# Kernel optimization log

Measured on AMD Instinct MI355X. Metric: run time of the kernel, lower is better.

## Reference

```python
import jax, jax.numpy as jnp
import numpy as np

K = 7          # kernel_size
PAD = 3        # padding
EPS = 1e-8


def setup_inputs() -> dict:
    key = jax.random.key(0)
    x = jax.random.normal(key, (32, 3, 512, 512), dtype=jnp.float32)
    return {"x": x}


def reference(x) -> jnp.ndarray:
    # Faithful fused version of: unfold -> center/neighbor cosine distance -> sum/8.
    # stride=1, dilation=1, padding=3, kernel=7 => output spatial size == input size,
    # and the patch center (flat index 24) is exactly the unpadded pixel itself.
    B, C, H, W = x.shape
    xp = jnp.pad(x, ((0, 0), (0, 0), (PAD, PAD), (PAD, PAD)))
    center = x  # == xp[:, :, PAD:PAD+H, PAD:PAD+W]
    # ||center|| over channels, clamped (matches .norm(dim=1).clamp_min(eps))
    cn = jnp.maximum(jnp.sqrt(jnp.sum(center * center, axis=1)), EPS)  # (B,H,W)
    acc = jnp.zeros((B, H, W), dtype=x.dtype)
    mid = K // 2
    for i in range(K):  # small fixed 7x7 loop; avoids materializing (B,C,49,H*W)
        for j in range(K):
            if i == mid and j == mid:
                continue  # skip center (neighbor_idx excludes center_flat)
            nb = xp[:, :, i:i + H, j:j + W]                      # (B,C,H,W)
            dot = jnp.sum(center * nb, axis=1)                   # (B,H,W)
            nn_ = jnp.maximum(jnp.sqrt(jnp.sum(nb * nb, axis=1)), EPS)
            acc = acc + (1.0 - dot / (cn * nn_))
    out = acc / 8.0  # module hardcodes /8 despite 48 neighbors
    return out[:, None, :, :]  # (B,1,H,W)
```

## Files before the change

### kernel.cpp

```cpp
#include <hip/hip_runtime.h>


typedef unsigned int u32;
typedef float f32x2 __attribute__((ext_vector_type(2)));
typedef float f32x4 __attribute__((ext_vector_type(4)));

#define EPS2 1e-16f

constexpr int HRN = 22;

__device__ __forceinline__ u32 packbf2(float a, float b) {
    const u32 ua = __float_as_uint(a) + 0x8000u;
    const u32 ub = __float_as_uint(b) + 0x8000u;
    return __builtin_amdgcn_perm(ub, ua, 0x07060302u);
}
__device__ __forceinline__ float uplo(u32 u) { return __uint_as_float(u << 16); }
__device__ __forceinline__ float uphi(u32 u) { return __uint_as_float(u & 0xffff0000u); }
__device__ __forceinline__ f32x2 up2(u32 u) {
    f32x2 r; r.x = uplo(u); r.y = uphi(u); return r;
}
__device__ __forceinline__ f32x4 vmul(f32x4 v, float s) {
    f32x4 r; r[0]=v[0]*s; r[1]=v[1]*s; r[2]=v[2]*s; r[3]=v[3]*s; return r;
}

__global__ __launch_bounds__(256, 3) void mcnd_kernel(const float* __restrict__ x,
                                                      float* __restrict__ out,
                                                      int B, int H, int W) {
    __shared__ uint4 hsh[4][3][HRN][8];

    const int HW = H * W;
    const int tilesX = W >> 6;
    const int tilesPerImg = tilesX * (H >> 6);

    const int cpx  = gridDim.x >> 3;
    const int wgid = (blockIdx.x & 7) * cpx + (blockIdx.x >> 3);
    const int b    = wgid / tilesPerImg;
    const int t    = wgid % tilesPerImg;
    const int ty   = t / tilesX;
    const int tx   = t - ty * tilesX;
    const int x0   = tx << 6;

    const int wv   = threadIdx.x >> 6;
    const int lane = threadIdx.x & 63;
    const int r2   = lane >> 3;
    const int grp  = lane & 7;
    const int yw   = (ty << 6) + (wv << 4);

    const float* __restrict__ xb = x + (size_t)b * 3 * HW;

    const int   gxl   = x0 + (grp << 3) - 4;
    const float lmask = (gxl >= 0) ? 1.f : 0.f;
    const float rmask = (gxl + 16 <= W) ? 1.f : 0.f;
    const int   gofL  = (gxl >= 0) ? gxl : 0;
    const int   gofR  = (gxl + 16 <= W) ? (gxl + 12) : (W - 4);

    u32 gA0[4], gA1[4], gA2[4];
    u32 gB0[4], gB1[4], gB2[4];
    uint4 hA[3], hB[3];

    auto process = [&](int hr, u32* cp0, u32* cp1, u32* cp2, uint4* hcap) {
        const int   gy  = yw + hr - 3;
        const float rmk = (gy >= 0 && gy < H) ? 1.f : 0.f;
        const int   gyc = gy < 0 ? 0 : (gy >= H ? H - 1 : gy);
        const float* rp0 = xb + (size_t)gyc * W;
        const float* rp1 = rp0 + HW;
        const float* rp2 = rp1 + HW;
        f32x4 a0 = *(const f32x4*)(rp0 + gofL);
        f32x4 a1 = *(const f32x4*)(rp0 + gxl + 4);
        f32x4 a2 = *(const f32x4*)(rp0 + gxl + 8);
        f32x4 a3 = *(const f32x4*)(rp0 + gofR);
        f32x4 b0 = *(const f32x4*)(rp1 + gofL);
        f32x4 b1 = *(const f32x4*)(rp1 + gxl + 4);
        f32x4 b2 = *(const f32x4*)(rp1 + gxl + 8);
        f32x4 b3 = *(const f32x4*)(rp1 + gofR);
        f32x4 c0 = *(const f32x4*)(rp2 + gofL);
        f32x4 c1 = *(const f32x4*)(rp2 + gxl + 4);
        f32x4 c2 = *(const f32x4*)(rp2 + gxl + 8);
        f32x4 c3 = *(const f32x4*)(rp2 + gofR);
        a0 = vmul(a0, lmask); b0 = vmul(b0, lmask); c0 = vmul(c0, lmask);
        a3 = vmul(a3, rmask); b3 = vmul(b3, rmask); c3 = vmul(c3, rmask);
        f32x4 i0, i1, i2, i3;
        {
            const f32x4 n0 = a0*a0 + b0*b0 + c0*c0;
            const f32x4 n1 = a1*a1 + b1*b1 + c1*c1;
            const f32x4 n2 = a2*a2 + b2*b2 + c2*c2;
            const f32x4 n3 = a3*a3 + b3*b3 + c3*c3;
#pragma unroll
            for (int e = 0; e < 4; ++e) {
                i0[e] = __builtin_amdgcn_rsqf(fmaxf(n0[e], EPS2)) * rmk;
                i1[e] = __builtin_amdgcn_rsqf(fmaxf(n1[e], EPS2)) * rmk;
                i2[e] = __builtin_amdgcn_rsqf(fmaxf(n2[e], EPS2)) * rmk;
                i3[e] = __builtin_amdgcn_rsqf(fmaxf(n3[e], EPS2)) * rmk;
            }
        }
        auto chan = [&](const f32x4& A0, const f32x4& A1, const f32x4& A2,
                        const f32x4& A3, int ch, u32* gcp, uint4* hc) {
            float cc[16];
#pragma unroll
            for (int e = 0; e < 4; ++e) {
                cc[e]      = A0[e] * i0[e];
                cc[4 + e]  = A1[e] * i1[e];
                cc[8 + e]  = A2[e] * i2[e];
                cc[12 + e] = A3[e] * i3[e];
            }
            float hp[8];
            hp[0] = cc[1]+cc[2]+cc[3]+cc[4]+cc[5]+cc[6]+cc[7];
#pragma unroll
            for (int m = 1; m < 8; ++m) hp[m] = hp[m-1] - cc[m] + cc[m+7];
            uint4 hwv;
            hwv.x = packbf2(hp[0], hp[1]); hwv.y = packbf2(hp[2], hp[3]);
            hwv.z = packbf2(hp[4], hp[5]); hwv.w = packbf2(hp[6], hp[7]);
            hsh[wv][ch][hr][grp] = hwv;
            if (hc) *hc = hwv;
            if (gcp) {
                gcp[0] = packbf2(cc[4],  cc[5]);
                gcp[1] = packbf2(cc[6],  cc[7]);
                gcp[2] = packbf2(cc[8],  cc[9]);
                gcp[3] = packbf2(cc[10], cc[11]);
            }
        };
        chan(a0, a1, a2, a3, 0, cp0, hcap ? &hcap[0] : nullptr);
        chan(b0, b1, b2, b3, 1, cp1, hcap ? &hcap[1] : nullptr);
        chan(c0, c1, c2, c3, 2, cp2, hcap ? &hcap[2] : nullptr);
    };

    process(2*r2 + 3, gA0, gA1, gA2, hA);
    process(2*r2 + 4, gB0, gB1, gB2, hB);
    if (lane < 48) {
        const int rr = lane >> 3;
        process(rr < 3 ? rr : rr + 16, nullptr, nullptr, nullptr, nullptr);
    }
    asm volatile("s_waitcnt lgkmcnt(0)" ::: "memory");
    __builtin_amdgcn_sched_barrier(0);

    f32x2 D0[4], D1[4];
#pragma unroll
    for (int e = 0; e < 4; ++e) { D0[e] = f32x2{0.f,0.f}; D1[e] = f32x2{0.f,0.f}; }
    auto vch = [&](int ch, const u32* ga, const u32* gb) {
        const uint4 u0 = hsh[wv][ch][2*r2][grp];
        f32x2 s0 = up2(u0.x), s1 = up2(u0.y), s2 = up2(u0.z), s3 = up2(u0.w);
#pragma unroll
        for (int d = 1; d < 3; ++d) {
            const uint4 u = hsh[wv][ch][2*r2 + d][grp];
            s0 += up2(u.x); s1 += up2(u.y); s2 += up2(u.z); s3 += up2(u.w);
        }
        s0 += up2(hA[ch].x) + up2(hB[ch].x);
        s1 += up2(hA[ch].y) + up2(hB[ch].y);
        s2 += up2(hA[ch].z) + up2(hB[ch].z);
        s3 += up2(hA[ch].w) + up2(hB[ch].w);
#pragma unroll
        for (int d = 5; d < 7; ++d) {
            const uint4 u = hsh[wv][ch][2*r2 + d][grp];
            s0 += up2(u.x); s1 += up2(u.y); s2 += up2(u.z); s3 += up2(u.w);
        }
        const uint4 u7 = hsh[wv][ch][2*r2 + 7][grp];
        D0[0] += up2(ga[0]) * s0;
        D0[1] += up2(ga[1]) * s1;
        D0[2] += up2(ga[2]) * s2;
        D0[3] += up2(ga[3]) * s3;
        D1[0] += up2(gb[0]) * (s0 - up2(u0.x) + up2(u7.x));
        D1[1] += up2(gb[1]) * (s1 - up2(u0.y) + up2(u7.y));
        D1[2] += up2(gb[2]) * (s2 - up2(u0.z) + up2(u7.z));
        D1[3] += up2(gb[3]) * (s3 - up2(u0.w) + up2(u7.w));
    };
    vch(0, gA0, gB0); vch(1, gA1, gB1); vch(2, gA2, gB2);

    f32x4 o00, o01, o10, o11;
#pragma unroll
    for (int e = 0; e < 4; ++e) {
        const f32x2 v0 = (f32x2{49.f, 49.f} - D0[e]) * 0.125f;
        const f32x2 v1 = (f32x2{49.f, 49.f} - D1[e]) * 0.125f;
        if (e < 2) { o00[2*e] = v0.x; o00[2*e+1] = v0.y;
                     o10[2*e] = v1.x; o10[2*e+1] = v1.y; }
        else       { o01[2*(e-2)] = v0.x; o01[2*(e-2)+1] = v0.y;
                     o11[2*(e-2)] = v1.x; o11[2*(e-2)+1] = v1.y; }
    }
    float* op = out + (size_t)b * HW + (size_t)(yw + 2*r2) * W + (x0 + (grp << 3));
    *(f32x4*)(op)         = o00;
    *(f32x4*)(op + 4)     = o01;
    *(f32x4*)(op + W)     = o10;
    *(f32x4*)(op + W + 4) = o11;
}

extern "C" void kernel_launch(void* const* d_in, const int* in_sizes, int n_in,
                              void* d_out, int out_size, void* d_ws, size_t ws_size,
                              hipStream_t stream) {
    (void)n_in; (void)d_ws; (void)ws_size; (void)out_size;
    const float* x = (const float*)d_in[0];
    float* out = (float*)d_out;

    const int H = 512, W = 512, C = 3;
    const int B = in_sizes[0] / (C * H * W);

    const int tilesPerImg = (W >> 6) * (H >> 6);
    mcnd_kernel<<<B * tilesPerImg, 256, 0, stream>>>(x, out, B, H, W);
}
```

Measured before the change: 31.09 us.

## Share vertical halo rows across waves via block-wide LDS buffer

```diff
diff --git a/kernel.cpp b/kernel.cpp
--- a/kernel.cpp
+++ b/kernel.cpp
@@ -6,8 +6,6 @@
 typedef float f32x4 __attribute__((ext_vector_type(4)));
 
 #define EPS2 1e-16f
-
-constexpr int HRN = 22;
 
 __device__ __forceinline__ u32 packbf2(float a, float b) {
     const u32 ua = __float_as_uint(a) + 0x8000u;
@@ -26,7 +24,7 @@
 __global__ __launch_bounds__(256, 3) void mcnd_kernel(const float* __restrict__ x,
                                                       float* __restrict__ out,
                                                       int B, int H, int W) {
-    __shared__ uint4 hsh[4][3][HRN][8];
+    __shared__ uint4 hsh[3][70][8];
 
     const int HW = H * W;
     const int tilesX = W >> 6;
@@ -39,12 +37,13 @@
     const int ty   = t / tilesX;
     const int tx   = t - ty * tilesX;
     const int x0   = tx << 6;
+    const int y0   = ty << 6;
 
     const int wv   = threadIdx.x >> 6;
     const int lane = threadIdx.x & 63;
     const int r2   = lane >> 3;
     const int grp  = lane & 7;
-    const int yw   = (ty << 6) + (wv << 4);
+    const int hw0  = (wv << 4) + 2*r2;
 
     const float* __restrict__ xb = x + (size_t)b * 3 * HW;
 
@@ -58,8 +57,8 @@
     u32 gB0[4], gB1[4], gB2[4];
     uint4 hA[3], hB[3];
 
-    auto process = [&](int hr, u32* cp0, u32* cp1, u32* cp2, uint4* hcap) {
-        const int   gy  = yw + hr - 3;
+    auto process = [&](int hh, u32* cp0, u32* cp1, u32* cp2, uint4* hcap) {
+        const int   gy  = y0 + hh - 3;
         const float rmk = (gy >= 0 && gy < H) ? 1.f : 0.f;
         const int   gyc = gy < 0 ? 0 : (gy >= H ? H - 1 : gy);
         const float* rp0 = xb + (size_t)gyc * W;
@@ -110,7 +109,7 @@
             uint4 hwv;
             hwv.x = packbf2(hp[0], hp[1]); hwv.y = packbf2(hp[2], hp[3]);
             hwv.z = packbf2(hp[4], hp[5]); hwv.w = packbf2(hp[6], hp[7]);
-            hsh[wv][ch][hr][grp] = hwv;
+            hsh[ch][hh][grp] = hwv;
             if (hc) *hc = hwv;
             if (gcp) {
                 gcp[0] = packbf2(cc[4],  cc[5]);
@@ -124,24 +123,23 @@
         chan(c0, c1, c2, c3, 2, cp2, hcap ? &hcap[2] : nullptr);
     };
 
-    process(2*r2 + 3, gA0, gA1, gA2, hA);
-    process(2*r2 + 4, gB0, gB1, gB2, hB);
-    if (lane < 48) {
+    process(hw0 + 3, gA0, gA1, gA2, hA);
+    process(hw0 + 4, gB0, gB1, gB2, hB);
+    if (threadIdx.x < 48) {
         const int rr = lane >> 3;
-        process(rr < 3 ? rr : rr + 16, nullptr, nullptr, nullptr, nullptr);
+        process(rr < 3 ? rr : rr + 64, nullptr, nullptr, nullptr, nullptr);
     }
-    asm volatile("s_waitcnt lgkmcnt(0)" ::: "memory");
-    __builtin_amdgcn_sched_barrier(0);
+    __syncthreads();
 
     f32x2 D0[4], D1[4];
 #pragma unroll
     for (int e = 0; e < 4; ++e) { D0[e] = f32x2{0.f,0.f}; D1[e] = f32x2{0.f,0.f}; }
     auto vch = [&](int ch, const u32* ga, const u32* gb) {
-        const uint4 u0 = hsh[wv][ch][2*r2][grp];
+        const uint4 u0 = hsh[ch][hw0][grp];
         f32x2 s0 = up2(u0.x), s1 = up2(u0.y), s2 = up2(u0.z), s3 = up2(u0.w);
 #pragma unroll
         for (int d = 1; d < 3; ++d) {
-            const uint4 u = hsh[wv][ch][2*r2 + d][grp];
+            const uint4 u = hsh[ch][hw0 + d][grp];
             s0 += up2(u.x); s1 += up2(u.y); s2 += up2(u.z); s3 += up2(u.w);
         }
         s0 += up2(hA[ch].x) + up2(hB[ch].x);
@@ -150,10 +148,10 @@
         s3 += up2(hA[ch].w) + up2(hB[ch].w);
 #pragma unroll
         for (int d = 5; d < 7; ++d) {
-            const uint4 u = hsh[wv][ch][2*r2 + d][grp];
+            const uint4 u = hsh[ch][hw0 + d][grp];
             s0 += up2(u.x); s1 += up2(u.y); s2 += up2(u.z); s3 += up2(u.w);
         }
-        const uint4 u7 = hsh[wv][ch][2*r2 + 7][grp];
+        const uint4 u7 = hsh[ch][hw0 + 7][grp];
         D0[0] += up2(ga[0]) * s0;
         D0[1] += up2(ga[1]) * s1;
         D0[2] += up2(ga[2]) * s2;
@@ -175,7 +173,7 @@
         else       { o01[2*(e-2)] = v0.x; o01[2*(e-2)+1] = v0.y;
                      o11[2*(e-2)] = v1.x; o11[2*(e-2)+1] = v1.y; }
     }
-    float* op = out + (size_t)b * HW + (size_t)(yw + 2*r2) * W + (x0 + (grp << 3));
+    float* op = out + (size_t)b * HW + (size_t)(y0 + hw0) * W + (x0 + (grp << 3));
     *(f32x4*)(op)         = o00;
     *(f32x4*)(op + 4)     = o01;
     *(f32x4*)(op + W)     = o10;
```

After: 32.66 us. 5.1% more time.
